# Optimization experiments

Hardware: AMD Instinct MI355X
Metric: run time of the kernel (lower is better)

The kernel has to match this reference:

```python
import jax, jax.numpy as jnp
import numpy as np


def setup_inputs() -> dict:
    key = jax.random.key(0)
    k1, k2, k3, k4, k5 = jax.random.split(key, 5)
    B, S, E, H, D = 8, 1024, 1024, 8, 128  # batch, seq, embed, heads, hidden/head
    stdv = 1.0 / np.sqrt(D)
    return {
        "k": jax.random.normal(k1, (B, S, E), jnp.float32),
        "q": jax.random.normal(k2, (B, S, E), jnp.float32),
        "flag": 0,  # False: project q through w_qx
        "w_kx": jax.random.uniform(k3, (H, E, D), jnp.float32, -stdv, stdv),
        "w_qx": jax.random.uniform(k4, (H, E, D), jnp.float32, -stdv, stdv),
        "proj_w": jax.random.normal(k5, (E, H * D), jnp.float32) * 0.02,  # out_dim = embed_dim
        "proj_b": jnp.zeros((E,), jnp.float32),
    }


def reference(k, q, flag, w_kx, w_qx, proj_w, proj_b):
    H, E, D = w_kx.shape
    B, Sk, _ = k.shape
    Sq = q.shape[1]
    # per-head tanh projections: [H, B, S, D]
    kx = jnp.tanh(jnp.einsum("bse,hed->hbsd", k, w_kx))
    if flag:
        qx = jnp.broadcast_to(q[None], (H,) + q.shape)  # q already in hidden space
    else:
        qx = jnp.tanh(jnp.einsum("bse,hed->hbsd", q, w_qx))
    # scaled dot product scores [H, B, Sq, Sk]
    score = jnp.einsum("hbqd,hbkd->hbqk", qx, kx) / jnp.sqrt(jnp.float32(D))
    attn = jax.nn.softmax(score, axis=-1)
    out = jnp.einsum("hbqk,hbkd->hbqd", attn, kx)  # [H, B, Sq, D]
    # concat heads: [B, Sq, H*D], then output projection (dropout p=0 is identity)
    out = jnp.transpose(out, (1, 2, 0, 3)).reshape(B, Sq, H * D)
    return out @ proj_w.T + proj_b
```

## Files before the change

kernel.cpp:

```cpp
#include <hip/hip_runtime.h>

typedef unsigned short u16;
typedef unsigned int u32;
typedef __bf16 bf16x8 __attribute__((ext_vector_type(8)));
typedef float f32x4 __attribute__((ext_vector_type(4)));

#define MFMA16(a, b, c) __builtin_amdgcn_mfma_f32_16x16x32_bf16(a, b, c, 0, 0, 0)
#define EXP2(x) __builtin_amdgcn_exp2f(x)

typedef const void __attribute__((address_space(1)))* gas1_t;
typedef void __attribute__((address_space(3)))* las3_t;

__device__ __forceinline__ void gload16(const void* g, void* l) {
  __builtin_amdgcn_global_load_lds((gas1_t)g, (las3_t)l, 16, 0, 0);
}

__device__ __forceinline__ u16 f2bf(float f) {
  union { float f; u32 u; } v; v.f = f;
  u32 r = v.u + 0x7FFFu + ((v.u >> 16) & 1u);
  return (u16)(r >> 16);
}

__device__ __forceinline__ float fast_tanh(float x) {
  float xc = fminf(fmaxf(x, -20.f), 20.f);
  float t = EXP2(xc * 2.885390081777927f);
  return (t - 1.0f) * __builtin_amdgcn_rcpf(t + 1.0f);
}

__global__ __launch_bounds__(256) void cvt_kernel(const float* __restrict__ in,
                                                  u16* __restrict__ out, int n8) {
  int i = blockIdx.x * blockDim.x + threadIdx.x;
  int stride = gridDim.x * blockDim.x;
  for (; i < n8; i += stride) {
    const float4* p = (const float4*)(in + (size_t)i * 8);
    float4 a = p[0], b = p[1];
    u16 t[8];
    t[0] = f2bf(a.x); t[1] = f2bf(a.y); t[2] = f2bf(a.z); t[3] = f2bf(a.w);
    t[4] = f2bf(b.x); t[5] = f2bf(b.y); t[6] = f2bf(b.z); t[7] = f2bf(b.w);
    *(uint4*)(out + (size_t)i * 8) = *(uint4*)t;
  }
}

__global__ __launch_bounds__(256) void wtrans_kernel(const float* __restrict__ w,
                                                     u16* __restrict__ wT) {
  __shared__ float t[64][65];
  int h = blockIdx.z;
  int e0 = blockIdx.x * 64, d0 = blockIdx.y * 64;
  const float* src = w + (size_t)h * 1024 * 128;
  u16* dst = wT + (size_t)h * 128 * 1024;
  int tid = threadIdx.x;
  {
    int row = tid >> 2, c0 = (tid & 3) * 16;
#pragma unroll
    for (int i = 0; i < 4; ++i) {
      float4 v = *(const float4*)(src + (size_t)(e0 + row) * 128 + d0 + c0 + i * 4);
      t[row][c0 + i * 4 + 0] = v.x;
      t[row][c0 + i * 4 + 1] = v.y;
      t[row][c0 + i * 4 + 2] = v.z;
      t[row][c0 + i * 4 + 3] = v.w;
    }
  }
  __syncthreads();
  {
    int dl = tid >> 2, c0 = (tid & 3) * 16;
    u16 tmp[16];
#pragma unroll
    for (int i = 0; i < 16; ++i) tmp[i] = f2bf(t[c0 + i][dl]);
    u16* o = dst + (size_t)(d0 + dl) * 1024 + e0 + c0;
    *(uint4*)o = *(uint4*)tmp;
    *(uint4*)(o + 8) = *(uint4*)(tmp + 8);
  }
}


template <int BM>
__device__ __forceinline__ void gemm8_core(const u16* __restrict__ Ab,
                                           const u16* __restrict__ Bb,
                                           int K, u16* lds,
                                           f32x4 (&acc)[BM / 32][4]) {
  constexpr int MH = BM / 64;
  constexpr int HR = BM / 4;
  constexpr int AH = (BM / 2) * 64;
  constexpr int BH = 128 * 64;
  constexpr int BUF = 2 * AH + 2 * BH;
  constexpr int LA = BM / 128;
  const int tid = threadIdx.x, lane = tid & 63, wid = tid >> 6;
  const int wr = wid >> 2, wc = wid & 3, l15 = lane & 15, g = lane >> 4;
  const int nkt = K >> 6;
  const int arow = wr * HR;
  const int brow = wc * 32;

  auto stageA = [&](u16* dstHalf, int mh, int kt) {
#pragma unroll
    for (int i = 0; i < LA; ++i) {
      int c = (wid * LA + i) * 64 + lane;
      int rr = c >> 3, src = (c & 7) ^ (rr & 7);
      int grow = (rr / HR) * (2 * HR) + mh * HR + (rr % HR);
      gload16((const char*)Ab + ((size_t)grow * K + kt * 64 + src * 8) * 2,
              (char*)dstHalf + c * 16);
    }
  };
  auto stageB = [&](u16* dstHalf, int nh, int kt) {
#pragma unroll
    for (int i = 0; i < 2; ++i) {
      int c = (wid * 2 + i) * 64 + lane;
      int cc = c >> 3, src = (c & 7) ^ (cc & 7);
      int gcol = (cc >> 5) * 64 + nh * 32 + (cc & 31);
      gload16((const char*)Bb + ((size_t)gcol * K + kt * 64 + src * 8) * 2,
              (char*)dstHalf + c * 16);
    }
  };

#define LDAF(half)                                                              \
  _Pragma("unroll") for (int m = 0; m < MH; ++m)                                \
  _Pragma("unroll") for (int kc = 0; kc < 2; ++kc) {                            \
    int r_ = arow + m * 16 + l15;                                               \
    af[m][kc] = *(const bf16x8*)((half) + r_ * 64 + (((kc * 4 + g) ^ (r_ & 7)) << 3)); \
  }
#define LDBF(half)                                                              \
  _Pragma("unroll") for (int n = 0; n < 2; ++n)                                 \
  _Pragma("unroll") for (int kc = 0; kc < 2; ++kc) {                            \
    int r_ = brow + n * 16 + l15;                                               \
    bb[n][kc] = *(const bf16x8*)((half) + r_ * 64 + (((kc * 4 + g) ^ (r_ & 7)) << 3)); \
  }
#define MFMAQ(MB, NB)                                                           \
  __builtin_amdgcn_s_setprio(1);                                                \
  _Pragma("unroll") for (int m = 0; m < MH; ++m)                                \
  _Pragma("unroll") for (int n = 0; n < 2; ++n)                                 \
  _Pragma("unroll") for (int kc = 0; kc < 2; ++kc)                              \
    acc[(MB) * MH + m][(NB) * 2 + n] =                                          \
        MFMA16(af[m][kc], bb[n][kc], acc[(MB) * MH + m][(NB) * 2 + n]);         \
  __builtin_amdgcn_s_setprio(0);

  stageA(lds, 0, 0);
  stageB(lds + 2 * AH, 0, 0);
  stageA(lds + AH, 1, 0);
  stageB(lds + 2 * AH + BH, 1, 0);
  if constexpr (BM == 256) asm volatile("s_waitcnt vmcnt(4)" ::: "memory");
  else                     asm volatile("s_waitcnt vmcnt(3)" ::: "memory");
  __builtin_amdgcn_s_barrier();

  bf16x8 af[MH][2], bb[2][2];
  for (int t = 0; t < nkt; ++t) {
    const int cur = t & 1;
    u16* A0c = lds + cur * BUF;
    u16* A1c = A0c + AH;
    u16* B0c = A0c + 2 * AH;
    u16* B1c = B0c + BH;
    u16* A0n = lds + (cur ^ 1) * BUF;
    u16* A1n = A0n + AH;
    u16* B0n = A0n + 2 * AH;
    u16* B1n = B0n + BH;
    const bool pf = (t + 1 < nkt);
    const int k1 = t + 1;

    asm volatile("s_waitcnt vmcnt(2)" ::: "memory");
    LDAF(A0c);
    LDBF(B0c);
    if (pf) stageA(A0n, 0, k1);
    __builtin_amdgcn_s_barrier();
    MFMAQ(0, 0);
    __builtin_amdgcn_s_barrier();

    if (pf) {
      if constexpr (BM == 256) asm volatile("s_waitcnt vmcnt(2)" ::: "memory");
      else                     asm volatile("s_waitcnt vmcnt(1)" ::: "memory");
    } else {
      asm volatile("s_waitcnt vmcnt(0)" ::: "memory");
    }
    LDAF(A1c);
    if (pf) stageB(B0n, 0, k1);
    __builtin_amdgcn_s_barrier();
    MFMAQ(1, 0);
    __builtin_amdgcn_s_barrier();

    LDBF(B1c);
    if (pf) stageA(A1n, 1, k1);
    __builtin_amdgcn_s_barrier();
    MFMAQ(1, 1);
    __builtin_amdgcn_s_barrier();

    if (pf) {
      if constexpr (BM == 256) asm volatile("s_waitcnt vmcnt(2)" ::: "memory");
      else                     asm volatile("s_waitcnt vmcnt(1)" ::: "memory");
    }
    LDAF(A0c);
    if (pf) stageB(B1n, 1, k1);
    __builtin_amdgcn_s_barrier();
    MFMAQ(0, 1);
    __builtin_amdgcn_s_barrier();
  }
#undef LDAF
#undef LDBF
#undef MFMAQ
}

__global__ __launch_bounds__(512, 2) void gemm_tanh_kernel(
    const u16* __restrict__ Ak, const u16* __restrict__ Aq,
    const u16* __restrict__ wTk, const u16* __restrict__ wTq,
    u16* __restrict__ kxo, u16* __restrict__ qxo) {
  __shared__ alignas(16) u16 lds[2 * (2 * 128 * 64 + 2 * 128 * 64)];
  const u16* A; const u16* W; u16* C;
  if (blockIdx.z == 0) { A = Ak; W = wTk; C = kxo; }
  else { A = Aq; W = wTq; C = qxo; }
  int mBase = blockIdx.x * 256;
  int nBase = blockIdx.y * 256;
  f32x4 acc[8][4];
#pragma unroll
  for (int i = 0; i < 8; ++i)
#pragma unroll
    for (int j = 0; j < 4; ++j) acc[i][j] = (f32x4){0.f, 0.f, 0.f, 0.f};
  gemm8_core<256>(A + (size_t)mBase * 1024, W + (size_t)nBase * 1024, 1024,
                  lds, acc);
  const int lane = threadIdx.x & 63, wid = threadIdx.x >> 6;
  const int wr = wid >> 2, wc = wid & 3, l15 = lane & 15, g = lane >> 4;
#pragma unroll
  for (int mf = 0; mf < 8; ++mf)
#pragma unroll
    for (int nf = 0; nf < 4; ++nf)
#pragma unroll
      for (int j = 0; j < 4; ++j) {
        int m = mBase + wr * 128 + mf * 16 + g * 4 + j;
        int n = nBase + wc * 64 + nf * 16 + l15;
        int h = n >> 7, d = n & 127;
        C[(size_t)h * 8192 * 128 + (size_t)m * 128 + d] =
            f2bf(fast_tanh(acc[mf][nf][j]));
      }
}

__global__ __launch_bounds__(256) void transpose_kernel(const u16* __restrict__ kx,
                                                        u16* __restrict__ kxT) {
  __shared__ u16 t[64][72];
  int hb = blockIdx.z;
  const u16* src = kx + (size_t)hb * 1024 * 128;
  u16* dst = kxT + (size_t)hb * 128 * 1024;
  int s0 = blockIdx.x * 64, d0 = blockIdx.y * 64;
  int tid = threadIdx.x;
#pragma unroll
  for (int r = 0; r < 2; ++r) {
    int row = r * 32 + (tid >> 3), c8 = (tid & 7) * 8;
    uint4 v = *(const uint4*)(src + (size_t)(s0 + row) * 128 + d0 + c8);
    *(uint4*)&t[row][c8] = v;
  }
  __syncthreads();
#pragma unroll
  for (int r = 0; r < 2; ++r) {
    int dl = r * 32 + (tid >> 3), s8 = (tid & 7) * 8;
    u16 tmp[8];
#pragma unroll
    for (int i = 0; i < 8; ++i) tmp[i] = t[s8 + i][dl];
    *(uint4*)(dst + (size_t)(d0 + dl) * 1024 + s0 + s8) = *(uint4*)tmp;
  }
}

__global__ __launch_bounds__(256, 2) void attn_kernel(const u16* __restrict__ qx,
                                                      const u16* __restrict__ kx,
                                                      const u16* __restrict__ kxT,
                                                      u16* __restrict__ X) {
  __shared__ alignas(16) u16 Klds[2][64 * 128];
  __shared__ alignas(16) u16 Vlds[2][128 * 64];
  __shared__ alignas(16) u16 Plds[4][32 * 64];
  const int tid = threadIdx.x, lane = tid & 63, wid = tid >> 6;
  const int g = lane >> 4;
  const int hb = blockIdx.x, qt = blockIdx.y, h = hb >> 3, b = hb & 7;
  const u16* qxh = qx + ((size_t)h * 8192 + (size_t)b * 1024) * 128;
  const u16* kxh = kx + ((size_t)h * 8192 + (size_t)b * 1024) * 128;
  const u16* kxTh = kxT + (size_t)hb * 128 * 1024;
  const int q0 = qt * 128 + wid * 32;
  const float SC = 0.08838834764831845f * 1.44269504088896340f;

#define STAGE(buf, kt_)                                                        \
  do {                                                                         \
    _Pragma("unroll") for (int i_ = 0; i_ < 4; ++i_) {                         \
      int cIdx = (wid * 4 + i_) * 64 + lane;                                   \
      {                                                                        \
        int row = cIdx >> 4, slot = cIdx & 15;                                 \
        int src = slot ^ (row & 7);                                            \
        gload16((const char*)kxh + (size_t)((kt_) * 64 + row) * 256 + src * 16,\
                (char*)&Klds[buf][0] + (wid * 4 + i_) * 1024);                 \
      }                                                                        \
      {                                                                        \
        int row = cIdx >> 3, slot = cIdx & 7;                                  \
        int src = slot ^ (row & 7);                                            \
        gload16((const char*)kxTh + (size_t)row * 2048 + (kt_) * 128 + src * 16,\
                (char*)&Vlds[buf][0] + (wid * 4 + i_) * 1024);                 \
      }                                                                        \
    }                                                                          \
  } while (0)

  bf16x8 qa[2][4];
#pragma unroll
  for (int m = 0; m < 2; ++m)
#pragma unroll
    for (int kc = 0; kc < 4; ++kc)
      qa[m][kc] = *(const bf16x8*)(qxh + (size_t)(q0 + m * 16 + (lane & 15)) * 128
                                   + kc * 32 + g * 8);

  f32x4 os[2][8];
#pragma unroll
  for (int i = 0; i < 2; ++i)
#pragma unroll
    for (int j = 0; j < 8; ++j) os[i][j] = (f32x4){0.f, 0.f, 0.f, 0.f};
  float lsum[2] = {0.f, 0.f};

  u16* Pw = &Plds[wid][0];

  STAGE(0, 0);

  for (int kt = 0; kt < 16; ++kt) {
    const int cur = kt & 1;
    if (kt < 15) {
      STAGE(cur ^ 1, kt + 1);
      asm volatile("s_waitcnt vmcnt(8)" ::: "memory");
    } else {
      asm volatile("s_waitcnt vmcnt(0)" ::: "memory");
    }
    __builtin_amdgcn_s_barrier();

    const u16* Kc = &Klds[cur][0];
    const u16* Vc = &Vlds[cur][0];

    f32x4 sa[4][2];
#pragma unroll
    for (int i = 0; i < 4; ++i)
#pragma unroll
      for (int j = 0; j < 2; ++j) sa[i][j] = (f32x4){0.f, 0.f, 0.f, 0.f};
    __builtin_amdgcn_s_setprio(1);
#pragma unroll
    for (int kc = 0; kc < 4; ++kc) {
      bf16x8 kb[4];
#pragma unroll
      for (int t = 0; t < 4; ++t) {
        int row = t * 16 + (lane & 15);
        int ch = kc * 4 + g;
        kb[t] = *(const bf16x8*)(Kc + row * 128 + ((ch ^ (row & 7)) << 3));
      }
#pragma unroll
      for (int t = 0; t < 4; ++t)
#pragma unroll
        for (int m = 0; m < 2; ++m)
          sa[t][m] = MFMA16(kb[t], qa[m][kc], sa[t][m]);
    }
    __builtin_amdgcn_s_setprio(0);

#pragma unroll
    for (int m = 0; m < 2; ++m) {
      int q = m * 16 + (lane & 15);
      int rowb = q * 128, q7 = q & 7;
#pragma unroll
      for (int t = 0; t < 4; ++t) {
        float p0 = EXP2(sa[t][m][0] * SC);
        float p1 = EXP2(sa[t][m][1] * SC);
        float p2 = EXP2(sa[t][m][2] * SC);
        float p3 = EXP2(sa[t][m][3] * SC);
        lsum[m] += (p0 + p1) + (p2 + p3);
        uint2 pk;
        pk.x = (u32)f2bf(p0) | ((u32)f2bf(p1) << 16);
        pk.y = (u32)f2bf(p2) | ((u32)f2bf(p3) << 16);
        int slot = (2 * t + (g >> 1)) ^ q7;
        *(uint2*)((char*)Pw + rowb + slot * 16 + 8 * (g & 1)) = pk;
      }
    }

    __builtin_amdgcn_s_setprio(1);
#pragma unroll
    for (int kc2 = 0; kc2 < 2; ++kc2) {
      bf16x8 pa[2], vb[8];
#pragma unroll
      for (int m = 0; m < 2; ++m) {
        int q = m * 16 + (lane & 15);
        int slot = (g + 4 * kc2) ^ (q & 7);
        pa[m] = *(const bf16x8*)((char*)Pw + q * 128 + slot * 16);
      }
#pragma unroll
      for (int nd = 0; nd < 8; ++nd) {
        int row = nd * 16 + (lane & 15);
        int ch = kc2 * 4 + g;
        vb[nd] = *(const bf16x8*)(Vc + row * 64 + ((ch ^ (row & 7)) << 3));
      }
#pragma unroll
      for (int m = 0; m < 2; ++m)
#pragma unroll
        for (int nd = 0; nd < 8; ++nd)
          os[m][nd] = MFMA16(pa[m], vb[nd], os[m][nd]);
    }
    __builtin_amdgcn_s_setprio(0);
    __builtin_amdgcn_s_barrier();
  }
#undef STAGE

#pragma unroll
  for (int m = 0; m < 2; ++m) {
    float s = lsum[m];
    s += __shfl_xor(s, 16);
    s += __shfl_xor(s, 32);
    lsum[m] = s;
  }

#pragma unroll
  for (int m = 0; m < 2; ++m)
#pragma unroll
    for (int j = 0; j < 4; ++j) {
      float tot = __shfl(lsum[m], 4 * g + j, 64);
      float inv = 1.f / tot;
      int qrow = b * 1024 + q0 + m * 16 + g * 4 + j;
#pragma unroll
      for (int nd = 0; nd < 8; ++nd) {
        int col = h * 128 + nd * 16 + (lane & 15);
        X[(size_t)qrow * 1024 + col] = f2bf(os[m][nd][j] * inv);
      }
    }
}

__global__ __launch_bounds__(512, 2) void gemm_bias_kernel(
    const u16* __restrict__ X, const u16* __restrict__ pw,
    const float* __restrict__ pb, float* __restrict__ out) {
  __shared__ alignas(16) u16 lds[2 * (2 * 64 * 64 + 2 * 128 * 64)];
  int mBase = blockIdx.x * 128;
  int nBase = blockIdx.y * 256;
  f32x4 acc[4][4];
#pragma unroll
  for (int i = 0; i < 4; ++i)
#pragma unroll
    for (int j = 0; j < 4; ++j) acc[i][j] = (f32x4){0.f, 0.f, 0.f, 0.f};
  gemm8_core<128>(X + (size_t)mBase * 1024, pw + (size_t)nBase * 1024, 1024,
                  lds, acc);
  const int lane = threadIdx.x & 63, wid = threadIdx.x >> 6;
  const int wr = wid >> 2, wc = wid & 3, l15 = lane & 15, g = lane >> 4;
#pragma unroll
  for (int nf = 0; nf < 4; ++nf) {
    int e = nBase + wc * 64 + nf * 16 + l15;
    float bv = pb[e];
#pragma unroll
    for (int mf = 0; mf < 4; ++mf)
#pragma unroll
      for (int j = 0; j < 4; ++j) {
        int m = mBase + wr * 64 + mf * 16 + g * 4 + j;
        out[(size_t)m * 1024 + e] = acc[mf][nf][j] + bv;
      }
  }
}

extern "C" void kernel_launch(void* const* d_in, const int* in_sizes, int n_in,
                              void* d_out, int out_size, void* d_ws, size_t ws_size,
                              hipStream_t stream) {
  const float* k = (const float*)d_in[0];
  const float* q = (const float*)d_in[1];
  const float* wk = (const float*)d_in[3];
  const float* wq = (const float*)d_in[4];
  const float* pw = (const float*)d_in[5];
  const float* pb = (const float*)d_in[6];
  float* out = (float*)d_out;
  char* ws = (char*)d_ws;

  u16* kbf = (u16*)(ws);
  u16* qbf = (u16*)(ws + (16ull << 20));
  u16* wTk = (u16*)(ws + (32ull << 20));
  u16* wTq = (u16*)(ws + (34ull << 20));
  u16* pwb = (u16*)(ws + (36ull << 20));
  u16* kx  = (u16*)(ws + (38ull << 20));
  u16* qx  = (u16*)(ws + (54ull << 20));
  u16* kxT = (u16*)(ws + (70ull << 20));
  u16* X   = kbf;

  cvt_kernel<<<2048, 256, 0, stream>>>(k, kbf, 1048576);
  cvt_kernel<<<2048, 256, 0, stream>>>(q, qbf, 1048576);
  cvt_kernel<<<512, 256, 0, stream>>>(pw, pwb, 131072);
  wtrans_kernel<<<dim3(16, 2, 8), 256, 0, stream>>>(wk, wTk);
  wtrans_kernel<<<dim3(16, 2, 8), 256, 0, stream>>>(wq, wTq);
  gemm_tanh_kernel<<<dim3(32, 4, 2), 512, 0, stream>>>(kbf, qbf, wTk, wTq, kx, qx);
  transpose_kernel<<<dim3(16, 2, 64), 256, 0, stream>>>(kx, kxT);
  attn_kernel<<<dim3(64, 8), 256, 0, stream>>>(qx, kx, kxT, X);
  gemm_bias_kernel<<<dim3(64, 4), 512, 0, stream>>>(X, pwb, pb, out);
}
```

Measured before the change: 137.5 us.

## Read K/V directly from global memory in attention, dropping LDS double-buffering

The attention kernel no longer stages K and V tiles into double-buffered shared memory with async global-to-LDS loads and barriers. Each wave now loads its MFMA operands straight from global memory, which frees shared memory and raises the occupancy hint from 2 to 3 blocks per CU. The cost is that all four waves in a block fetch the same K/V tiles separately, so they depend on L1/L2 reuse, and the loads are no longer prefetched ahead of the compute. The GEMM staging also now passes a wave-uniform LDS base address to the global-to-LDS loads instead of a per-lane address.

```diff
diff --git a/kernel.cpp b/kernel.cpp
--- a/kernel.cpp
+++ b/kernel.cpp
@@ -71,7 +71,6 @@
     *(uint4*)(o + 8) = *(uint4*)(tmp + 8);
   }
 }
-
 
 template <int BM>
 __device__ __forceinline__ void gemm8_core(const u16* __restrict__ Ab,
@@ -97,7 +96,7 @@
       int rr = c >> 3, src = (c & 7) ^ (rr & 7);
       int grow = (rr / HR) * (2 * HR) + mh * HR + (rr % HR);
       gload16((const char*)Ab + ((size_t)grow * K + kt * 64 + src * 8) * 2,
-              (char*)dstHalf + c * 16);
+              (char*)dstHalf + (wid * LA + i) * 1024);
     }
   };
   auto stageB = [&](u16* dstHalf, int nh, int kt) {
@@ -107,7 +106,7 @@
       int cc = c >> 3, src = (c & 7) ^ (cc & 7);
       int gcol = (cc >> 5) * 64 + nh * 32 + (cc & 31);
       gload16((const char*)Bb + ((size_t)gcol * K + kt * 64 + src * 8) * 2,
-              (char*)dstHalf + c * 16);
+              (char*)dstHalf + (wid * 2 + i) * 1024);
     }
   };
 
@@ -253,15 +252,13 @@
   }
 }
 
-__global__ __launch_bounds__(256, 2) void attn_kernel(const u16* __restrict__ qx,
+__global__ __launch_bounds__(256, 3) void attn_kernel(const u16* __restrict__ qx,
                                                       const u16* __restrict__ kx,
                                                       const u16* __restrict__ kxT,
                                                       u16* __restrict__ X) {
-  __shared__ alignas(16) u16 Klds[2][64 * 128];
-  __shared__ alignas(16) u16 Vlds[2][128 * 64];
   __shared__ alignas(16) u16 Plds[4][32 * 64];
   const int tid = threadIdx.x, lane = tid & 63, wid = tid >> 6;
-  const int g = lane >> 4;
+  const int g = lane >> 4, l15 = lane & 15;
   const int hb = blockIdx.x, qt = blockIdx.y, h = hb >> 3, b = hb & 7;
   const u16* qxh = qx + ((size_t)h * 8192 + (size_t)b * 1024) * 128;
   const u16* kxh = kx + ((size_t)h * 8192 + (size_t)b * 1024) * 128;
@@ -269,31 +266,12 @@
   const int q0 = qt * 128 + wid * 32;
   const float SC = 0.08838834764831845f * 1.44269504088896340f;
 
-#define STAGE(buf, kt_)                                                        \
-  do {                                                                         \
-    _Pragma("unroll") for (int i_ = 0; i_ < 4; ++i_) {                         \
-      int cIdx = (wid * 4 + i_) * 64 + lane;                                   \
-      {                                                                        \
-        int row = cIdx >> 4, slot = cIdx & 15;                                 \
-        int src = slot ^ (row & 7);                                            \
-        gload16((const char*)kxh + (size_t)((kt_) * 64 + row) * 256 + src * 16,\
-                (char*)&Klds[buf][0] + (wid * 4 + i_) * 1024);                 \
-      }                                                                        \
-      {                                                                        \
-        int row = cIdx >> 3, slot = cIdx & 7;                                  \
-        int src = slot ^ (row & 7);                                            \
-        gload16((const char*)kxTh + (size_t)row * 2048 + (kt_) * 128 + src * 16,\
-                (char*)&Vlds[buf][0] + (wid * 4 + i_) * 1024);                 \
-      }                                                                        \
-    }                                                                          \
-  } while (0)
-
   bf16x8 qa[2][4];
 #pragma unroll
   for (int m = 0; m < 2; ++m)
 #pragma unroll
     for (int kc = 0; kc < 4; ++kc)
-      qa[m][kc] = *(const bf16x8*)(qxh + (size_t)(q0 + m * 16 + (lane & 15)) * 128
+      qa[m][kc] = *(const bf16x8*)(qxh + (size_t)(q0 + m * 16 + l15) * 128
                                    + kc * 32 + g * 8);
 
   f32x4 os[2][8];
@@ -305,47 +283,29 @@
 
   u16* Pw = &Plds[wid][0];
 
-  STAGE(0, 0);
-
   for (int kt = 0; kt < 16; ++kt) {
-    const int cur = kt & 1;
-    if (kt < 15) {
-      STAGE(cur ^ 1, kt + 1);
-      asm volatile("s_waitcnt vmcnt(8)" ::: "memory");
-    } else {
-      asm volatile("s_waitcnt vmcnt(0)" ::: "memory");
-    }
-    __builtin_amdgcn_s_barrier();
-
-    const u16* Kc = &Klds[cur][0];
-    const u16* Vc = &Vlds[cur][0];
-
     f32x4 sa[4][2];
 #pragma unroll
     for (int i = 0; i < 4; ++i)
 #pragma unroll
       for (int j = 0; j < 2; ++j) sa[i][j] = (f32x4){0.f, 0.f, 0.f, 0.f};
-    __builtin_amdgcn_s_setprio(1);
 #pragma unroll
     for (int kc = 0; kc < 4; ++kc) {
       bf16x8 kb[4];
 #pragma unroll
-      for (int t = 0; t < 4; ++t) {
-        int row = t * 16 + (lane & 15);
-        int ch = kc * 4 + g;
-        kb[t] = *(const bf16x8*)(Kc + row * 128 + ((ch ^ (row & 7)) << 3));
-      }
+      for (int t = 0; t < 4; ++t)
+        kb[t] = *(const bf16x8*)(kxh + (size_t)(kt * 64 + t * 16 + l15) * 128
+                                 + kc * 32 + g * 8);
 #pragma unroll
       for (int t = 0; t < 4; ++t)
 #pragma unroll
         for (int m = 0; m < 2; ++m)
           sa[t][m] = MFMA16(kb[t], qa[m][kc], sa[t][m]);
     }
-    __builtin_amdgcn_s_setprio(0);
 
 #pragma unroll
     for (int m = 0; m < 2; ++m) {
-      int q = m * 16 + (lane & 15);
+      int q = m * 16 + l15;
       int rowb = q * 128, q7 = q & 7;
 #pragma unroll
       for (int t = 0; t < 4; ++t) {
@@ -362,32 +322,26 @@
       }
     }
 
-    __builtin_amdgcn_s_setprio(1);
 #pragma unroll
     for (int kc2 = 0; kc2 < 2; ++kc2) {
       bf16x8 pa[2], vb[8];
 #pragma unroll
       for (int m = 0; m < 2; ++m) {
-        int q = m * 16 + (lane & 15);
+        int q = m * 16 + l15;
         int slot = (g + 4 * kc2) ^ (q & 7);
         pa[m] = *(const bf16x8*)((char*)Pw + q * 128 + slot * 16);
       }
 #pragma unroll
-      for (int nd = 0; nd < 8; ++nd) {
-        int row = nd * 16 + (lane & 15);
-        int ch = kc2 * 4 + g;
-        vb[nd] = *(const bf16x8*)(Vc + row * 64 + ((ch ^ (row & 7)) << 3));
-      }
+      for (int nd = 0; nd < 8; ++nd)
+        vb[nd] = *(const bf16x8*)(kxTh + (size_t)(nd * 16 + l15) * 1024
+                                  + kt * 64 + kc2 * 32 + g * 8);
 #pragma unroll
       for (int m = 0; m < 2; ++m)
 #pragma unroll
         for (int nd = 0; nd < 8; ++nd)
           os[m][nd] = MFMA16(pa[m], vb[nd], os[m][nd]);
     }
-    __builtin_amdgcn_s_setprio(0);
-    __builtin_amdgcn_s_barrier();
-  }
-#undef STAGE
+  }
 
 #pragma unroll
   for (int m = 0; m < 2; ++m) {
@@ -406,7 +360,7 @@
       int qrow = b * 1024 + q0 + m * 16 + g * 4 + j;
 #pragma unroll
       for (int nd = 0; nd < 8; ++nd) {
-        int col = h * 128 + nd * 16 + (lane & 15);
+        int col = h * 128 + nd * 16 + l15;
         X[(size_t)qrow * 1024 + col] = f2bf(os[m][nd][j] * inv);
       }
     }
```

Result: slower. 213.2 us (+55.0%).
